# Performance work log

Hardware: AMD Instinct MI355X
Metric: run time of the kernel (lower is better)

## Reference

```python
import jax, jax.numpy as jnp
import numpy as np

N_NODES = 200000
N_EDGES = 6400000
IN_CH, HID_CH, OUT_CH = 128, 15, 32


def setup_inputs() -> dict:
    key = jax.random.key(0)
    k_x, k_e, k_w1, k_w2 = jax.random.split(key, 4)
    x = jax.random.normal(k_x, (N_NODES, IN_CH), dtype=jnp.float32)
    edge_index = jax.random.randint(k_e, (2, N_EDGES), 0, N_NODES, dtype=jnp.int64)
    # Glorot-style init for GCN weights
    W1 = jax.random.normal(k_w1, (IN_CH, HID_CH), dtype=jnp.float32) / np.sqrt(IN_CH)
    b1 = jnp.zeros((HID_CH,), dtype=jnp.float32)
    W2 = jax.random.normal(k_w2, (HID_CH, OUT_CH), dtype=jnp.float32) / np.sqrt(HID_CH)
    b2 = jnp.zeros((OUT_CH,), dtype=jnp.float32)
    return {"x": x, "edge_index": edge_index, "W1": W1, "b1": b1, "W2": W2, "b2": b2}


def _gcn_conv(x, src, dst, W, b, num_nodes):
    """PyG GCNConv: linear transform, symmetric-normalized scatter aggregate, bias.

    src/dst already include self-loops. Norm = deg^-1/2[src] * deg^-1/2[dst]
    with deg computed over target (dst) indices using unit edge weights.
    """
    deg = jax.ops.segment_sum(jnp.ones_like(dst, dtype=x.dtype), dst,
                              num_segments=num_nodes)
    dinv = jnp.where(deg > 0, jax.lax.rsqrt(deg), 0.0)  # deg_inv_sqrt, inf -> 0
    norm = dinv[src] * dinv[dst]                         # [E_total]
    h = x @ W                                            # [N, out] small GEMM first
    msg = h[src] * norm[:, None]                         # gather + per-edge scale
    out = jax.ops.segment_sum(msg, dst, num_segments=num_nodes)  # scatter-add
    return out + b


def reference(x, edge_index, W1, b1, W2, b2):
    num_nodes = x.shape[0]
    loops = jnp.arange(num_nodes, dtype=edge_index.dtype)
    src = jnp.concatenate([edge_index[0], loops])  # add self-loops (PyG default)
    dst = jnp.concatenate([edge_index[1], loops])
    h = jax.nn.relu(_gcn_conv(x, src, dst, W1, b1, num_nodes))
    return _gcn_conv(h, src, dst, W2, b2, num_nodes)
```

## Files before the change

### kernel.cpp

```cpp
#include <hip/hip_runtime.h>

#define N_IN   128
#define N_HID  15
#define N_HIDP 16
#define N_OUT  32

#define NBLK1  1024
#define QSHIFT 9
#define QNODES 512
#define QMAXQ  2048

__global__ void detect_kernel(const int* __restrict__ idx, int* __restrict__ flag) {
    __shared__ int nz;
    if (threadIdx.x == 0) nz = 0;
    __syncthreads();
    if (idx[2 * threadIdx.x + 1] != 0) atomicOr(&nz, 1);
    __syncthreads();
    if (threadIdx.x == 0) *flag = (nz == 0) ? 1 : 0;
}

__global__ __launch_bounds__(256) void hist_kernel(
    const void* __restrict__ idx, int E, const int* __restrict__ flag,
    unsigned* __restrict__ ghist, int NQ) {
    __shared__ unsigned h[QMAXQ];
    for (int q = threadIdx.x; q < NQ; q += 256) h[q] = 0u;
    __syncthreads();
    const bool is64 = (*flag != 0);
    const long long* p64 = (const long long*)idx;
    const int*       p32 = (const int*)idx;
    const int epb = (E + NBLK1 - 1) / NBLK1;
    const int lo = blockIdx.x * epb;
    const int hi = min(lo + epb, E);
    for (int e = lo + threadIdx.x; e < hi; e += 256) {
        int d = is64 ? (int)p64[E + e] : p32[E + e];
        atomicAdd(&h[d >> QSHIFT], 1u);
    }
    __syncthreads();
    for (int q = threadIdx.x; q < NQ; q += 256)
        ghist[(size_t)q * NBLK1 + blockIdx.x] = h[q];
}

__global__ void scanA_kernel(unsigned* __restrict__ a, unsigned* __restrict__ bsum) {
    __shared__ unsigned sh[256];
    int t = threadIdx.x;
    size_t base = (size_t)blockIdx.x * 1024 + t * 4;
    unsigned d0 = a[base], d1 = a[base + 1], d2 = a[base + 2], d3 = a[base + 3];
    unsigned tot = d0 + d1 + d2 + d3;
    sh[t] = tot;
    __syncthreads();
    for (int off = 1; off < 256; off <<= 1) {
        unsigned v = (t >= off) ? sh[t - off] : 0u;
        __syncthreads();
        sh[t] += v;
        __syncthreads();
    }
    unsigned ex = sh[t] - tot;
    if (t == 255) bsum[blockIdx.x] = sh[255];
    a[base] = ex;
    a[base + 1] = ex + d0;
    a[base + 2] = ex + d0 + d1;
    a[base + 3] = ex + d0 + d1 + d2;
}

__global__ void scanB_kernel(unsigned* __restrict__ bsum, int nb) {
    __shared__ unsigned sh[256];
    int t = threadIdx.x;
    unsigned v0 = (2 * t < nb) ? bsum[2 * t] : 0u;
    unsigned v1 = (2 * t + 1 < nb) ? bsum[2 * t + 1] : 0u;
    unsigned tot = v0 + v1;
    sh[t] = tot;
    __syncthreads();
    for (int off = 1; off < 256; off <<= 1) {
        unsigned v = (t >= off) ? sh[t - off] : 0u;
        __syncthreads();
        sh[t] += v;
        __syncthreads();
    }
    unsigned ex = sh[t] - tot;
    if (2 * t < nb) bsum[2 * t] = ex;
    if (2 * t + 1 < nb) bsum[2 * t + 1] = ex + v0;
}

__global__ __launch_bounds__(256) void place_kernel(
    const void* __restrict__ idx, int E, const int* __restrict__ flag,
    const unsigned* __restrict__ goff, const unsigned* __restrict__ bsum,
    unsigned* __restrict__ grecs, int NQ) {
    __shared__ unsigned cur[QMAXQ];
    for (int q = threadIdx.x; q < NQ; q += 256)
        cur[q] = goff[(size_t)q * NBLK1 + blockIdx.x] + bsum[q];
    __syncthreads();
    const bool is64 = (*flag != 0);
    const long long* p64 = (const long long*)idx;
    const int*       p32 = (const int*)idx;
    const int epb = (E + NBLK1 - 1) / NBLK1;
    const int lo = blockIdx.x * epb;
    const int hi = min(lo + epb, E);
    for (int e = lo + threadIdx.x; e < hi; e += 256) {
        int s, d;
        if (is64) { s = (int)p64[e]; d = (int)p64[E + e]; }
        else      { s = p32[e];      d = p32[E + e]; }
        unsigned pos = atomicAdd(&cur[d >> QSHIFT], 1u);
        grecs[pos] = ((unsigned)s << QSHIFT) | (unsigned)(d & (QNODES - 1));
    }
}

__global__ __launch_bounds__(256) void build_kernel(
    const unsigned* __restrict__ grecs, const unsigned* __restrict__ bsum,
    int E, int N, int NQ, unsigned* __restrict__ rowst,
    unsigned* __restrict__ deg, float* __restrict__ dinv,
    int* __restrict__ srcs) {
    __shared__ unsigned dl[QNODES];
    __shared__ unsigned rl[QNODES];
    __shared__ unsigned cnt[QNODES];
    __shared__ unsigned sc[256];
    const int q = blockIdx.x;
    const int lo = q << QSHIFT;
    const int nn = min(QNODES, N - lo);
    const unsigned rbase = bsum[q];
    const unsigned rend  = (q + 1 < NQ) ? bsum[q + 1] : (unsigned)E;
    const int t = threadIdx.x;
    dl[2 * t] = 0u; dl[2 * t + 1] = 0u;
    cnt[2 * t] = 0u; cnt[2 * t + 1] = 0u;
    __syncthreads();
    for (unsigned i = rbase + t; i < rend; i += 256)
        atomicAdd(&dl[grecs[i] & (QNODES - 1u)], 1u);
    __syncthreads();
    unsigned d0 = dl[2 * t], d1 = dl[2 * t + 1];
    unsigned tot = d0 + d1;
    sc[t] = tot;
    __syncthreads();
    for (int off = 1; off < 256; off <<= 1) {
        unsigned v = (t >= off) ? sc[t - off] : 0u;
        __syncthreads();
        sc[t] += v;
        __syncthreads();
    }
    unsigned ex = sc[t] - tot;
    rl[2 * t]     = rbase + ex;
    rl[2 * t + 1] = rbase + ex + d0;
    if (2 * t < nn) {
        rowst[lo + 2 * t] = rl[2 * t];
        deg[lo + 2 * t] = d0;
        dinv[lo + 2 * t] = rsqrtf((float)d0 + 1.0f);
    }
    if (2 * t + 1 < nn) {
        rowst[lo + 2 * t + 1] = rl[2 * t + 1];
        deg[lo + 2 * t + 1] = d1;
        dinv[lo + 2 * t + 1] = rsqrtf((float)d1 + 1.0f);
    }
    __syncthreads();
    for (unsigned i = rbase + t; i < rend; i += 256) {
        unsigned rec = grecs[i];
        unsigned l = rec & (QNODES - 1u);
        unsigned pos = rl[l] + atomicAdd(&cnt[l], 1u);
        srcs[pos] = (int)(rec >> QSHIFT);
    }
}

__global__ __launch_bounds__(256) void gemm1_kernel(
    const float* __restrict__ x, const float* __restrict__ W1,
    const float* __restrict__ dinv, float* __restrict__ hs, int N) {
    __shared__ float Wl[N_IN * N_HIDP];
    for (int i = threadIdx.x; i < N_IN * N_HIDP; i += 256) {
        int k = i >> 4, c = i & 15;
        Wl[i] = (c < N_HID) ? W1[k * N_HID + c] : 0.f;
    }
    __syncthreads();
    const float4* __restrict__ Wl4 = (const float4*)Wl;
    const float4* __restrict__ x4  = (const float4*)x;

    int r0 = blockIdx.x * 512 + threadIdx.x;
    int r1 = r0 + 256;
    int r0c = r0 < N ? r0 : N - 1;
    int r1c = r1 < N ? r1 : N - 1;

    float acc0[16], acc1[16];
#pragma unroll
    for (int c = 0; c < 16; ++c) { acc0[c] = 0.f; acc1[c] = 0.f; }

    for (int k4 = 0; k4 < 32; ++k4) {
        float4 xv0 = x4[r0c * 32 + k4];
        float4 xv1 = x4[r1c * 32 + k4];
        float xs0[4] = {xv0.x, xv0.y, xv0.z, xv0.w};
        float xs1[4] = {xv1.x, xv1.y, xv1.z, xv1.w};
#pragma unroll
        for (int t = 0; t < 4; ++t) {
            int k = k4 * 4 + t;
            float4 wa = Wl4[k * 4 + 0];
            float4 wb = Wl4[k * 4 + 1];
            float4 wc = Wl4[k * 4 + 2];
            float4 wd = Wl4[k * 4 + 3];
            float wf[16] = {wa.x, wa.y, wa.z, wa.w, wb.x, wb.y, wb.z, wb.w,
                            wc.x, wc.y, wc.z, wc.w, wd.x, wd.y, wd.z, wd.w};
#pragma unroll
            for (int c = 0; c < 16; ++c) {
                acc0[c] = fmaf(xs0[t], wf[c], acc0[c]);
                acc1[c] = fmaf(xs1[t], wf[c], acc1[c]);
            }
        }
    }
    float4* __restrict__ hs4 = (float4*)hs;
    if (r0 < N) {
        float di = dinv[r0];
#pragma unroll
        for (int j = 0; j < 4; ++j)
            hs4[r0 * 4 + j] = make_float4(acc0[4*j]*di, acc0[4*j+1]*di,
                                          acc0[4*j+2]*di, acc0[4*j+3]*di);
    }
    if (r1 < N) {
        float di = dinv[r1];
#pragma unroll
        for (int j = 0; j < 4; ++j)
            hs4[r1 * 4 + j] = make_float4(acc1[4*j]*di, acc1[4*j+1]*di,
                                          acc1[4*j+2]*di, acc1[4*j+3]*di);
    }
}

__global__ __launch_bounds__(256) void agg1_kernel(
    const int* __restrict__ srcs, const unsigned* __restrict__ rowst,
    const unsigned* __restrict__ deg, const float* __restrict__ hs,
    const float* __restrict__ dinv, const float* __restrict__ b1,
    float* __restrict__ hs2, int N) {
    int node = blockIdx.x * 4 + (threadIdx.x >> 6);
    if (node >= N) return;
    int lane = threadIdx.x & 63;
    int k = lane >> 4, c = lane & 15;
    unsigned dg = deg[node];
    unsigned base = rowst[node];
    float self = hs[(size_t)node * N_HIDP + c];
    float di = dinv[node];
    float acc = 0.f;
    unsigned t = k;
    for (; t + 28 < dg; t += 32) {
        int s[8];
#pragma unroll
        for (int j = 0; j < 8; ++j) s[j] = srcs[base + t + 4 * j];
        float v[8];
#pragma unroll
        for (int j = 0; j < 8; ++j) v[j] = hs[(size_t)s[j] * N_HIDP + c];
        acc += ((v[0] + v[1]) + (v[2] + v[3])) + ((v[4] + v[5]) + (v[6] + v[7]));
    }
    for (; t + 12 < dg; t += 16) {
        int s0 = srcs[base + t];
        int s1 = srcs[base + t + 4];
        int s2 = srcs[base + t + 8];
        int s3 = srcs[base + t + 12];
        float v0 = hs[(size_t)s0 * N_HIDP + c];
        float v1 = hs[(size_t)s1 * N_HIDP + c];
        float v2 = hs[(size_t)s2 * N_HIDP + c];
        float v3 = hs[(size_t)s3 * N_HIDP + c];
        acc += (v0 + v1) + (v2 + v3);
    }
    for (; t < dg; t += 4)
        acc += hs[(size_t)srcs[base + t] * N_HIDP + c];
    acc += __shfl_xor(acc, 16);
    acc += __shfl_xor(acc, 32);
    if (k == 0) {
        float b = (c < N_HID) ? b1[c] : 0.f;
        float v = fmaxf(di * (acc + self) + b, 0.f);
        hs2[(size_t)node * N_HIDP + c] = v * di;
    }
}

__global__ __launch_bounds__(256) void agg2_kernel(
    const int* __restrict__ srcs, const unsigned* __restrict__ rowst,
    const unsigned* __restrict__ deg, const float* __restrict__ hs2,
    const float* __restrict__ dinv, const float* __restrict__ W2,
    const float* __restrict__ b2, float* __restrict__ out, int N) {
    __shared__ float W2l[N_HID * N_OUT];
    for (int t = threadIdx.x; t < N_HID * N_OUT; t += 256) W2l[t] = W2[t];
    __syncthreads();
    int node = blockIdx.x * 4 + (threadIdx.x >> 6);
    if (node >= N) return;
    int lane = threadIdx.x & 63;
    int k = lane >> 4, c = lane & 15;
    unsigned dg = deg[node];
    unsigned base = rowst[node];
    float self = hs2[(size_t)node * N_HIDP + c];
    float di = dinv[node];
    float acc = 0.f;
    unsigned t = k;
    for (; t + 28 < dg; t += 32) {
        int s[8];
#pragma unroll
        for (int j = 0; j < 8; ++j) s[j] = srcs[base + t + 4 * j];
        float v[8];
#pragma unroll
        for (int j = 0; j < 8; ++j) v[j] = hs2[(size_t)s[j] * N_HIDP + c];
        acc += ((v[0] + v[1]) + (v[2] + v[3])) + ((v[4] + v[5]) + (v[6] + v[7]));
    }
    for (; t + 12 < dg; t += 16) {
        int s0 = srcs[base + t];
        int s1 = srcs[base + t + 4];
        int s2 = srcs[base + t + 8];
        int s3 = srcs[base + t + 12];
        float v0 = hs2[(size_t)s0 * N_HIDP + c];
        float v1 = hs2[(size_t)s1 * N_HIDP + c];
        float v2 = hs2[(size_t)s2 * N_HIDP + c];
        float v3 = hs2[(size_t)s3 * N_HIDP + c];
        acc += (v0 + v1) + (v2 + v3);
    }
    for (; t < dg; t += 4)
        acc += hs2[(size_t)srcs[base + t] * N_HIDP + c];
    acc += __shfl_xor(acc, 16);
    acc += __shfl_xor(acc, 32);
    float u = di * (acc + self);
    int j = lane & 31;
    float a = b2[j];
#pragma unroll
    for (int kk = 0; kk < N_HID; ++kk)
        a = fmaf(__shfl(u, kk), W2l[kk * N_OUT + j], a);
    if (lane < 32) out[(size_t)node * N_OUT + j] = a;
}

extern "C" void kernel_launch(void* const* d_in, const int* in_sizes, int n_in,
                              void* d_out, int out_size, void* d_ws, size_t ws_size,
                              hipStream_t stream) {
    const float* x   = (const float*)d_in[0];
    const void*  eix = d_in[1];
    const float* W1  = (const float*)d_in[2];
    const float* b1  = (const float*)d_in[3];
    const float* W2  = (const float*)d_in[4];
    const float* b2  = (const float*)d_in[5];
    float* out = (float*)d_out;

    const int N = in_sizes[0] / N_IN;
    const int E = in_sizes[1] / 2;
    const int NQ = (N + QNODES - 1) >> QSHIFT;

    char* ws = (char*)d_ws;
    size_t off = 0;
    auto alloc = [&](size_t bytes) -> void* {
        void* p = ws + off;
        off += (bytes + 255) & ~(size_t)255;
        return p;
    };
    unsigned* goff  = (unsigned*)alloc((size_t)NQ * NBLK1 * 4);
    unsigned* bsum  = (unsigned*)alloc((size_t)NQ * 4);
    unsigned* rowst = (unsigned*)alloc((size_t)N * 4);
    unsigned* deg   = (unsigned*)alloc((size_t)N * 4);
    float*    dinv  = (float*)alloc((size_t)N * 4);
    int*      srcs  = (int*)alloc((size_t)E * 4);
    float*    hs    = (float*)alloc((size_t)N * N_HIDP * 4);
    float*    hs2   = (float*)alloc((size_t)N * N_HIDP * 4);
    int*      flag  = (int*)alloc(256);
    unsigned* grecs = (unsigned*)hs;

    detect_kernel<<<1, 256, 0, stream>>>((const int*)eix, flag);

    hist_kernel<<<NBLK1, 256, 0, stream>>>(eix, E, flag, goff, NQ);
    scanA_kernel<<<NQ, 256, 0, stream>>>(goff, bsum);
    scanB_kernel<<<1, 256, 0, stream>>>(bsum, NQ);
    place_kernel<<<NBLK1, 256, 0, stream>>>(eix, E, flag, goff, bsum, grecs, NQ);
    build_kernel<<<NQ, 256, 0, stream>>>(grecs, bsum, E, N, NQ, rowst, deg, dinv, srcs);

    gemm1_kernel<<<(N + 511) / 512, 256, 0, stream>>>(x, W1, dinv, hs, N);
    agg1_kernel<<<(N + 3) / 4, 256, 0, stream>>>(srcs, rowst, deg, hs, dinv, b1, hs2, N);
    agg2_kernel<<<(N + 3) / 4, 256, 0, stream>>>(srcs, rowst, deg, hs2, dinv, W2, b2, out, N);
}
```

Baseline: 642.7 us.

## Store hidden features in fp16, widen CSR build blocks, unroll edge loops

Hidden features hs and hs2 are now stored as fp16, which halves gather traffic in the two aggregation kernels. Accumulation stays in fp32, but rounding error is added to the results. The histogram, placement and CSR build kernels use 512-thread blocks with half as many blocks and unroll the edge loops four ways to keep more loads in flight. The separate degree array is dropped and degree is derived from rowst[node+1]-rowst[node]. Buffers are rearranged so grecs gets its own allocation and hs/hs2 alias it.

```diff
diff --git a/kernel.cpp b/kernel.cpp
--- a/kernel.cpp
+++ b/kernel.cpp
@@ -5,7 +5,9 @@
 #define N_HIDP 16
 #define N_OUT  32
 
-#define NBLK1  1024
+typedef _Float16 half8 __attribute__((ext_vector_type(8)));
+
+#define NBLK1  512
 #define QSHIFT 9
 #define QNODES 512
 #define QMAXQ  2048
@@ -19,11 +21,11 @@
     if (threadIdx.x == 0) *flag = (nz == 0) ? 1 : 0;
 }
 
-__global__ __launch_bounds__(256) void hist_kernel(
+__global__ __launch_bounds__(512) void hist_kernel(
     const void* __restrict__ idx, int E, const int* __restrict__ flag,
     unsigned* __restrict__ ghist, int NQ) {
     __shared__ unsigned h[QMAXQ];
-    for (int q = threadIdx.x; q < NQ; q += 256) h[q] = 0u;
+    for (int q = threadIdx.x; q < NQ; q += 512) h[q] = 0u;
     __syncthreads();
     const bool is64 = (*flag != 0);
     const long long* p64 = (const long long*)idx;
@@ -31,21 +33,32 @@
     const int epb = (E + NBLK1 - 1) / NBLK1;
     const int lo = blockIdx.x * epb;
     const int hi = min(lo + epb, E);
-    for (int e = lo + threadIdx.x; e < hi; e += 256) {
+    int e = lo + threadIdx.x;
+    for (; e + 1536 < hi; e += 2048) {
+        int d0 = is64 ? (int)p64[E + e]        : p32[E + e];
+        int d1 = is64 ? (int)p64[E + e + 512]  : p32[E + e + 512];
+        int d2 = is64 ? (int)p64[E + e + 1024] : p32[E + e + 1024];
+        int d3 = is64 ? (int)p64[E + e + 1536] : p32[E + e + 1536];
+        atomicAdd(&h[d0 >> QSHIFT], 1u);
+        atomicAdd(&h[d1 >> QSHIFT], 1u);
+        atomicAdd(&h[d2 >> QSHIFT], 1u);
+        atomicAdd(&h[d3 >> QSHIFT], 1u);
+    }
+    for (; e < hi; e += 512) {
         int d = is64 ? (int)p64[E + e] : p32[E + e];
         atomicAdd(&h[d >> QSHIFT], 1u);
     }
     __syncthreads();
-    for (int q = threadIdx.x; q < NQ; q += 256)
+    for (int q = threadIdx.x; q < NQ; q += 512)
         ghist[(size_t)q * NBLK1 + blockIdx.x] = h[q];
 }
 
 __global__ void scanA_kernel(unsigned* __restrict__ a, unsigned* __restrict__ bsum) {
     __shared__ unsigned sh[256];
     int t = threadIdx.x;
-    size_t base = (size_t)blockIdx.x * 1024 + t * 4;
-    unsigned d0 = a[base], d1 = a[base + 1], d2 = a[base + 2], d3 = a[base + 3];
-    unsigned tot = d0 + d1 + d2 + d3;
+    size_t base = (size_t)blockIdx.x * NBLK1 + t * 2;
+    unsigned d0 = a[base], d1 = a[base + 1];
+    unsigned tot = d0 + d1;
     sh[t] = tot;
     __syncthreads();
     for (int off = 1; off < 256; off <<= 1) {
@@ -58,8 +71,6 @@
     if (t == 255) bsum[blockIdx.x] = sh[255];
     a[base] = ex;
     a[base + 1] = ex + d0;
-    a[base + 2] = ex + d0 + d1;
-    a[base + 3] = ex + d0 + d1 + d2;
 }
 
 __global__ void scanB_kernel(unsigned* __restrict__ bsum, int nb) {
@@ -81,12 +92,12 @@
     if (2 * t + 1 < nb) bsum[2 * t + 1] = ex + v0;
 }
 
-__global__ __launch_bounds__(256) void place_kernel(
+__global__ __launch_bounds__(512) void place_kernel(
     const void* __restrict__ idx, int E, const int* __restrict__ flag,
     const unsigned* __restrict__ goff, const unsigned* __restrict__ bsum,
     unsigned* __restrict__ grecs, int NQ) {
     __shared__ unsigned cur[QMAXQ];
-    for (int q = threadIdx.x; q < NQ; q += 256)
+    for (int q = threadIdx.x; q < NQ; q += 512)
         cur[q] = goff[(size_t)q * NBLK1 + blockIdx.x] + bsum[q];
     __syncthreads();
     const bool is64 = (*flag != 0);
@@ -95,7 +106,30 @@
     const int epb = (E + NBLK1 - 1) / NBLK1;
     const int lo = blockIdx.x * epb;
     const int hi = min(lo + epb, E);
-    for (int e = lo + threadIdx.x; e < hi; e += 256) {
+    int e = lo + threadIdx.x;
+    for (; e + 1536 < hi; e += 2048) {
+        int s0, d0, s1, d1, s2, d2, s3, d3;
+        if (is64) {
+            s0 = (int)p64[e];        d0 = (int)p64[E + e];
+            s1 = (int)p64[e + 512];  d1 = (int)p64[E + e + 512];
+            s2 = (int)p64[e + 1024]; d2 = (int)p64[E + e + 1024];
+            s3 = (int)p64[e + 1536]; d3 = (int)p64[E + e + 1536];
+        } else {
+            s0 = p32[e];        d0 = p32[E + e];
+            s1 = p32[e + 512];  d1 = p32[E + e + 512];
+            s2 = p32[e + 1024]; d2 = p32[E + e + 1024];
+            s3 = p32[e + 1536]; d3 = p32[E + e + 1536];
+        }
+        unsigned pos0 = atomicAdd(&cur[d0 >> QSHIFT], 1u);
+        unsigned pos1 = atomicAdd(&cur[d1 >> QSHIFT], 1u);
+        unsigned pos2 = atomicAdd(&cur[d2 >> QSHIFT], 1u);
+        unsigned pos3 = atomicAdd(&cur[d3 >> QSHIFT], 1u);
+        grecs[pos0] = ((unsigned)s0 << QSHIFT) | (unsigned)(d0 & (QNODES - 1));
+        grecs[pos1] = ((unsigned)s1 << QSHIFT) | (unsigned)(d1 & (QNODES - 1));
+        grecs[pos2] = ((unsigned)s2 << QSHIFT) | (unsigned)(d2 & (QNODES - 1));
+        grecs[pos3] = ((unsigned)s3 << QSHIFT) | (unsigned)(d3 & (QNODES - 1));
+    }
+    for (; e < hi; e += 512) {
         int s, d;
         if (is64) { s = (int)p64[e]; d = (int)p64[E + e]; }
         else      { s = p32[e];      d = p32[E + e]; }
@@ -104,62 +138,75 @@
     }
 }
 
-__global__ __launch_bounds__(256) void build_kernel(
+__global__ __launch_bounds__(512) void build_kernel(
     const unsigned* __restrict__ grecs, const unsigned* __restrict__ bsum,
     int E, int N, int NQ, unsigned* __restrict__ rowst,
-    unsigned* __restrict__ deg, float* __restrict__ dinv,
-    int* __restrict__ srcs) {
+    float* __restrict__ dinv, int* __restrict__ srcs) {
     __shared__ unsigned dl[QNODES];
     __shared__ unsigned rl[QNODES];
     __shared__ unsigned cnt[QNODES];
-    __shared__ unsigned sc[256];
+    __shared__ unsigned sc[QNODES];
     const int q = blockIdx.x;
     const int lo = q << QSHIFT;
     const int nn = min(QNODES, N - lo);
     const unsigned rbase = bsum[q];
     const unsigned rend  = (q + 1 < NQ) ? bsum[q + 1] : (unsigned)E;
     const int t = threadIdx.x;
-    dl[2 * t] = 0u; dl[2 * t + 1] = 0u;
-    cnt[2 * t] = 0u; cnt[2 * t + 1] = 0u;
-    __syncthreads();
-    for (unsigned i = rbase + t; i < rend; i += 256)
+    dl[t] = 0u; cnt[t] = 0u;
+    __syncthreads();
+    unsigned i = rbase + t;
+    for (; i + 1536 < rend; i += 2048) {
+        unsigned r0 = grecs[i], r1 = grecs[i + 512];
+        unsigned r2 = grecs[i + 1024], r3 = grecs[i + 1536];
+        atomicAdd(&dl[r0 & (QNODES - 1u)], 1u);
+        atomicAdd(&dl[r1 & (QNODES - 1u)], 1u);
+        atomicAdd(&dl[r2 & (QNODES - 1u)], 1u);
+        atomicAdd(&dl[r3 & (QNODES - 1u)], 1u);
+    }
+    for (; i < rend; i += 512)
         atomicAdd(&dl[grecs[i] & (QNODES - 1u)], 1u);
     __syncthreads();
-    unsigned d0 = dl[2 * t], d1 = dl[2 * t + 1];
-    unsigned tot = d0 + d1;
-    sc[t] = tot;
-    __syncthreads();
-    for (int off = 1; off < 256; off <<= 1) {
+    unsigned d = dl[t];
+    sc[t] = d;
+    __syncthreads();
+    for (int off = 1; off < 512; off <<= 1) {
         unsigned v = (t >= off) ? sc[t - off] : 0u;
         __syncthreads();
         sc[t] += v;
         __syncthreads();
     }
-    unsigned ex = sc[t] - tot;
-    rl[2 * t]     = rbase + ex;
-    rl[2 * t + 1] = rbase + ex + d0;
-    if (2 * t < nn) {
-        rowst[lo + 2 * t] = rl[2 * t];
-        deg[lo + 2 * t] = d0;
-        dinv[lo + 2 * t] = rsqrtf((float)d0 + 1.0f);
-    }
-    if (2 * t + 1 < nn) {
-        rowst[lo + 2 * t + 1] = rl[2 * t + 1];
-        deg[lo + 2 * t + 1] = d1;
-        dinv[lo + 2 * t + 1] = rsqrtf((float)d1 + 1.0f);
-    }
-    __syncthreads();
-    for (unsigned i = rbase + t; i < rend; i += 256) {
-        unsigned rec = grecs[i];
-        unsigned l = rec & (QNODES - 1u);
+    unsigned ex = sc[t] - d;
+    rl[t] = rbase + ex;
+    if (t < nn) {
+        rowst[lo + t] = rl[t];
+        dinv[lo + t] = rsqrtf((float)d + 1.0f);
+    }
+    if (q == NQ - 1 && t == 0) rowst[N] = (unsigned)E;
+    __syncthreads();
+    i = rbase + t;
+    for (; i + 1536 < rend; i += 2048) {
+        unsigned r0 = grecs[i], r1 = grecs[i + 512];
+        unsigned r2 = grecs[i + 1024], r3 = grecs[i + 1536];
+        unsigned p0 = rl[r0 & (QNODES - 1u)] + atomicAdd(&cnt[r0 & (QNODES - 1u)], 1u);
+        unsigned p1 = rl[r1 & (QNODES - 1u)] + atomicAdd(&cnt[r1 & (QNODES - 1u)], 1u);
+        unsigned p2 = rl[r2 & (QNODES - 1u)] + atomicAdd(&cnt[r2 & (QNODES - 1u)], 1u);
+        unsigned p3 = rl[r3 & (QNODES - 1u)] + atomicAdd(&cnt[r3 & (QNODES - 1u)], 1u);
+        srcs[p0] = (int)(r0 >> QSHIFT);
+        srcs[p1] = (int)(r1 >> QSHIFT);
+        srcs[p2] = (int)(r2 >> QSHIFT);
+        srcs[p3] = (int)(r3 >> QSHIFT);
+    }
+    for (; i < rend; i += 512) {
+        unsigned r = grecs[i];
+        unsigned l = r & (QNODES - 1u);
         unsigned pos = rl[l] + atomicAdd(&cnt[l], 1u);
-        srcs[pos] = (int)(rec >> QSHIFT);
+        srcs[pos] = (int)(r >> QSHIFT);
     }
 }
 
 __global__ __launch_bounds__(256) void gemm1_kernel(
     const float* __restrict__ x, const float* __restrict__ W1,
-    const float* __restrict__ dinv, float* __restrict__ hs, int N) {
+    const float* __restrict__ dinv, _Float16* __restrict__ hs, int N) {
     __shared__ float Wl[N_IN * N_HIDP];
     for (int i = threadIdx.x; i < N_IN * N_HIDP; i += 256) {
         int k = i >> 4, c = i & 15;
@@ -199,35 +246,41 @@
             }
         }
     }
-    float4* __restrict__ hs4 = (float4*)hs;
     if (r0 < N) {
         float di = dinv[r0];
-#pragma unroll
-        for (int j = 0; j < 4; ++j)
-            hs4[r0 * 4 + j] = make_float4(acc0[4*j]*di, acc0[4*j+1]*di,
-                                          acc0[4*j+2]*di, acc0[4*j+3]*di);
+        half8 h0, h1;
+#pragma unroll
+        for (int j = 0; j < 8; ++j) {
+            h0[j] = (_Float16)(acc0[j] * di);
+            h1[j] = (_Float16)(acc0[8 + j] * di);
+        }
+        *(half8*)(hs + (size_t)r0 * N_HIDP) = h0;
+        *(half8*)(hs + (size_t)r0 * N_HIDP + 8) = h1;
     }
     if (r1 < N) {
         float di = dinv[r1];
-#pragma unroll
-        for (int j = 0; j < 4; ++j)
-            hs4[r1 * 4 + j] = make_float4(acc1[4*j]*di, acc1[4*j+1]*di,
-                                          acc1[4*j+2]*di, acc1[4*j+3]*di);
+        half8 h0, h1;
+#pragma unroll
+        for (int j = 0; j < 8; ++j) {
+            h0[j] = (_Float16)(acc1[j] * di);
+            h1[j] = (_Float16)(acc1[8 + j] * di);
+        }
+        *(half8*)(hs + (size_t)r1 * N_HIDP) = h0;
+        *(half8*)(hs + (size_t)r1 * N_HIDP + 8) = h1;
     }
 }
 
 __global__ __launch_bounds__(256) void agg1_kernel(
     const int* __restrict__ srcs, const unsigned* __restrict__ rowst,
-    const unsigned* __restrict__ deg, const float* __restrict__ hs,
-    const float* __restrict__ dinv, const float* __restrict__ b1,
-    float* __restrict__ hs2, int N) {
+    const _Float16* __restrict__ hs, const float* __restrict__ dinv,
+    const float* __restrict__ b1, _Float16* __restrict__ hs2, int N) {
     int node = blockIdx.x * 4 + (threadIdx.x >> 6);
     if (node >= N) return;
     int lane = threadIdx.x & 63;
     int k = lane >> 4, c = lane & 15;
-    unsigned dg = deg[node];
     unsigned base = rowst[node];
-    float self = hs[(size_t)node * N_HIDP + c];
+    unsigned dg = rowst[node + 1] - base;
+    float self = (float)hs[(size_t)node * N_HIDP + c];
     float di = dinv[node];
     float acc = 0.f;
     unsigned t = k;
@@ -237,7 +290,7 @@
         for (int j = 0; j < 8; ++j) s[j] = srcs[base + t + 4 * j];
         float v[8];
 #pragma unroll
-        for (int j = 0; j < 8; ++j) v[j] = hs[(size_t)s[j] * N_HIDP + c];
+        for (int j = 0; j < 8; ++j) v[j] = (float)hs[(size_t)s[j] * N_HIDP + c];
         acc += ((v[0] + v[1]) + (v[2] + v[3])) + ((v[4] + v[5]) + (v[6] + v[7]));
     }
     for (; t + 12 < dg; t += 16) {
@@ -245,28 +298,28 @@
         int s1 = srcs[base + t + 4];
         int s2 = srcs[base + t + 8];
         int s3 = srcs[base + t + 12];
-        float v0 = hs[(size_t)s0 * N_HIDP + c];
-        float v1 = hs[(size_t)s1 * N_HIDP + c];
-        float v2 = hs[(size_t)s2 * N_HIDP + c];
-        float v3 = hs[(size_t)s3 * N_HIDP + c];
+        float v0 = (float)hs[(size_t)s0 * N_HIDP + c];
+        float v1 = (float)hs[(size_t)s1 * N_HIDP + c];
+        float v2 = (float)hs[(size_t)s2 * N_HIDP + c];
+        float v3 = (float)hs[(size_t)s3 * N_HIDP + c];
         acc += (v0 + v1) + (v2 + v3);
     }
     for (; t < dg; t += 4)
-        acc += hs[(size_t)srcs[base + t] * N_HIDP + c];
+        acc += (float)hs[(size_t)srcs[base + t] * N_HIDP + c];
     acc += __shfl_xor(acc, 16);
     acc += __shfl_xor(acc, 32);
     if (k == 0) {
         float b = (c < N_HID) ? b1[c] : 0.f;
         float v = fmaxf(di * (acc + self) + b, 0.f);
-        hs2[(size_t)node * N_HIDP + c] = v * di;
+        hs2[(size_t)node * N_HIDP + c] = (_Float16)(v * di);
     }
 }
 
 __global__ __launch_bounds__(256) void agg2_kernel(
     const int* __restrict__ srcs, const unsigned* __restrict__ rowst,
-    const unsigned* __restrict__ deg, const float* __restrict__ hs2,
-    const float* __restrict__ dinv, const float* __restrict__ W2,
-    const float* __restrict__ b2, float* __restrict__ out, int N) {
+    const _Float16* __restrict__ hs2, const float* __restrict__ dinv,
+    const float* __restrict__ W2, const float* __restrict__ b2,
+    float* __restrict__ out, int N) {
     __shared__ float W2l[N_HID * N_OUT];
     for (int t = threadIdx.x; t < N_HID * N_OUT; t += 256) W2l[t] = W2[t];
     __syncthreads();
@@ -274,9 +327,9 @@
     if (node >= N) return;
     int lane = threadIdx.x & 63;
     int k = lane >> 4, c = lane & 15;
-    unsigned dg = deg[node];
     unsigned base = rowst[node];
-    float self = hs2[(size_t)node * N_HIDP + c];
+    unsigned dg = rowst[node + 1] - base;
+    float self = (float)hs2[(size_t)node * N_HIDP + c];
     float di = dinv[node];
     float acc = 0.f;
     unsigned t = k;
@@ -286,7 +339,7 @@
         for (int j = 0; j < 8; ++j) s[j] = srcs[base + t + 4 * j];
         float v[8];
 #pragma unroll
-        for (int j = 0; j < 8; ++j) v[j] = hs2[(size_t)s[j] * N_HIDP + c];
+        for (int j = 0; j < 8; ++j) v[j] = (float)hs2[(size_t)s[j] * N_HIDP + c];
         acc += ((v[0] + v[1]) + (v[2] + v[3])) + ((v[4] + v[5]) + (v[6] + v[7]));
     }
     for (; t + 12 < dg; t += 16) {
@@ -294,14 +347,14 @@
         int s1 = srcs[base + t + 4];
         int s2 = srcs[base + t + 8];
         int s3 = srcs[base + t + 12];
-        float v0 = hs2[(size_t)s0 * N_HIDP + c];
-        float v1 = hs2[(size_t)s1 * N_HIDP + c];
-        float v2 = hs2[(size_t)s2 * N_HIDP + c];
-        float v3 = hs2[(size_t)s3 * N_HIDP + c];
+        float v0 = (float)hs2[(size_t)s0 * N_HIDP + c];
+        float v1 = (float)hs2[(size_t)s1 * N_HIDP + c];
+        float v2 = (float)hs2[(size_t)s2 * N_HIDP + c];
+        float v3 = (float)hs2[(size_t)s3 * N_HIDP + c];
         acc += (v0 + v1) + (v2 + v3);
     }
     for (; t < dg; t += 4)
-        acc += hs2[(size_t)srcs[base + t] * N_HIDP + c];
+        acc += (float)hs2[(size_t)srcs[base + t] * N_HIDP + c];
     acc += __shfl_xor(acc, 16);
     acc += __shfl_xor(acc, 32);
     float u = di * (acc + self);
@@ -337,24 +390,23 @@
     };
     unsigned* goff  = (unsigned*)alloc((size_t)NQ * NBLK1 * 4);
     unsigned* bsum  = (unsigned*)alloc((size_t)NQ * 4);
-    unsigned* rowst = (unsigned*)alloc((size_t)N * 4);
-    unsigned* deg   = (unsigned*)alloc((size_t)N * 4);
+    unsigned* rowst = (unsigned*)alloc((size_t)(N + 1) * 4);
     float*    dinv  = (float*)alloc((size_t)N * 4);
     int*      srcs  = (int*)alloc((size_t)E * 4);
-    float*    hs    = (float*)alloc((size_t)N * N_HIDP * 4);
-    float*    hs2   = (float*)alloc((size_t)N * N_HIDP * 4);
+    unsigned* grecs = (unsigned*)alloc((size_t)E * 4);
     int*      flag  = (int*)alloc(256);
-    unsigned* grecs = (unsigned*)hs;
+    _Float16* hs  = (_Float16*)grecs;
+    _Float16* hs2 = hs + (size_t)N * N_HIDP;
 
     detect_kernel<<<1, 256, 0, stream>>>((const int*)eix, flag);
 
-    hist_kernel<<<NBLK1, 256, 0, stream>>>(eix, E, flag, goff, NQ);
+    hist_kernel<<<NBLK1, 512, 0, stream>>>(eix, E, flag, goff, NQ);
     scanA_kernel<<<NQ, 256, 0, stream>>>(goff, bsum);
     scanB_kernel<<<1, 256, 0, stream>>>(bsum, NQ);
-    place_kernel<<<NBLK1, 256, 0, stream>>>(eix, E, flag, goff, bsum, grecs, NQ);
-    build_kernel<<<NQ, 256, 0, stream>>>(grecs, bsum, E, N, NQ, rowst, deg, dinv, srcs);
+    place_kernel<<<NBLK1, 512, 0, stream>>>(eix, E, flag, goff, bsum, grecs, NQ);
+    build_kernel<<<NQ, 512, 0, stream>>>(grecs, bsum, E, N, NQ, rowst, dinv, srcs);
 
     gemm1_kernel<<<(N + 511) / 512, 256, 0, stream>>>(x, W1, dinv, hs, N);
-    agg1_kernel<<<(N + 3) / 4, 256, 0, stream>>>(srcs, rowst, deg, hs, dinv, b1, hs2, N);
-    agg2_kernel<<<(N + 3) / 4, 256, 0, stream>>>(srcs, rowst, deg, hs2, dinv, W2, b2, out, N);
-}
+    agg1_kernel<<<(N + 3) / 4, 256, 0, stream>>>(srcs, rowst, hs, dinv, b1, hs2, N);
+    agg2_kernel<<<(N + 3) / 4, 256, 0, stream>>>(srcs, rowst, hs2, dinv, W2, b2, out, N);
+}
```

Result: faster. 560.1 us (-12.8%).
